# Optimization experiments

Measured on AMD Instinct MI355X. Metric: run time of the kernel, lower is better.

## Reference

```python
import jax, jax.numpy as jnp
import numpy as np

B, S, D, H = 1, 4096, 1024, 16
HD = D // H  # head_dim = 64
NEG = -1e9


def _rotate_half(x):
    x1, x2 = jnp.split(x, 2, axis=-1)
    return jnp.concatenate([-x2, x1], axis=-1)


def _apply_rope(x, cos, sin):
    # x: [b, s, h, hd]; cos/sin: [s, hd] -> broadcast over batch and heads
    c = cos[None, :, None, :]
    s = sin[None, :, None, :]
    return x * c + _rotate_half(x) * s


def setup_inputs() -> dict:
    key = jax.random.key(0)
    kx, kq, ko = jax.random.split(key, 3)
    x = jax.random.normal(kx, (B, S, D), dtype=jnp.float32)
    # causal additive mask (finite large-negative for safe grads)
    i = jnp.arange(S)
    attn_mask = jnp.where(i[None, :] > i[:, None], NEG, 0.0).astype(jnp.float32)[None, None]
    # standard RoPE tables
    inv_freq = 1.0 / (10000.0 ** (np.arange(0, HD, 2, dtype=np.float32) / HD))
    ang = np.arange(S, dtype=np.float32)[:, None] * inv_freq[None, :]  # [S, HD/2]
    ang = np.concatenate([ang, ang], axis=-1)  # [S, HD]
    rope_cos = jnp.asarray(np.cos(ang))
    rope_sin = jnp.asarray(np.sin(ang))
    W_qkv = jax.random.normal(kq, (D, 3 * D), dtype=jnp.float32) * (D ** -0.5)
    W_out = jax.random.normal(ko, (D, D), dtype=jnp.float32) * (D ** -0.5)
    return {"x": x, "attn_mask": attn_mask, "rope_cos": rope_cos,
            "rope_sin": rope_sin, "W_qkv": W_qkv, "W_out": W_out}


def reference(x, attn_mask, rope_cos, rope_sin, W_qkv, W_out):
    b, s, d = x.shape
    qkv = x @ W_qkv                              # [b, s, 3d]
    q, k, v = jnp.split(qkv, 3, axis=-1)
    q = q.reshape(b, s, H, HD)
    k = k.reshape(b, s, H, HD)
    v = v.reshape(b, s, H, HD)
    q = _apply_rope(q, rope_cos, rope_sin)
    k = _apply_rope(k, rope_cos, rope_sin)
    att = jnp.einsum('bqhd,bkhd->bhqk', q, k) / jnp.sqrt(jnp.float32(HD))
    att = att + attn_mask                        # additive mask broadcast [b,h,s,s]
    att = jax.nn.softmax(att, axis=-1)
    out = jnp.einsum('bhqk,bkhd->bqhd', att, v).reshape(b, s, d)
    return out @ W_out
```

## Files before the change

### kernel.cpp

```cpp
#include <hip/hip_runtime.h>


typedef __attribute__((ext_vector_type(8)))  __bf16 bf16x8;
typedef __attribute__((ext_vector_type(4)))  float  f32x4;
typedef __attribute__((ext_vector_type(16))) float  f32x16;
typedef __attribute__((ext_vector_type(8)))  unsigned short ushort8;
typedef __attribute__((ext_vector_type(4)))  unsigned int   u32x4;

#define MFMA16(a,b,c) __builtin_amdgcn_mfma_f32_16x16x32_bf16((a),(b),(c),0,0,0)
#define MFMA32(a,b,c) __builtin_amdgcn_mfma_f32_32x32x16_bf16((a),(b),(c),0,0,0)

static __device__ __forceinline__ unsigned short f2bf(float f) {
  unsigned int u = __builtin_bit_cast(unsigned int, f);
  u = (u + 0x7FFFu + ((u >> 16) & 1u)) >> 16;
  return (unsigned short)u;
}
static __device__ __forceinline__ float bf2f(unsigned short u) {
  return __builtin_bit_cast(float, (unsigned int)u << 16);
}
static __device__ __forceinline__ unsigned int cvtpk(float a, float b) {
  unsigned int r;
  asm("v_cvt_pk_bf16_f32 %0, %1, %2" : "=v"(r) : "v"(a), "v"(b));
  return r;
}
static __device__ __forceinline__ void plswap(unsigned int& a, unsigned int& b) {
#if __has_builtin(__builtin_amdgcn_permlane32_swap)
  auto r = __builtin_amdgcn_permlane32_swap(a, b, false, false);
  a = r[0]; b = r[1];
#else
  unsigned int xa = (unsigned int)__shfl_xor((int)a, 32);
  unsigned int xb = (unsigned int)__shfl_xor((int)b, 32);
  int lane = __builtin_amdgcn_mbcnt_hi(~0u, __builtin_amdgcn_mbcnt_lo(~0u, 0));
  bool hi = lane >= 32;
  a = hi ? xb : a;
  b = hi ? b : xa;
#endif
}
static __device__ __forceinline__ void gll16(const unsigned short* gp, const unsigned short* lp) {
  unsigned int m0v = __builtin_amdgcn_readfirstlane((unsigned int)(unsigned long long)(uintptr_t)lp);
  asm volatile("s_mov_b32 m0, %0\n\tglobal_load_lds_dwordx4 %1, off"
               :: "s"(m0v), "v"(gp) : "memory");
}
static __device__ __forceinline__ void wait_dma() {
  asm volatile("s_waitcnt vmcnt(0)" ::: "memory");
}

__global__ void convert_x(const float* __restrict__ x, unsigned short* __restrict__ o) {
  int i = (blockIdx.x * 256 + threadIdx.x) * 4;
  float4 v = *reinterpret_cast<const float4*>(x + i);
  ushort4 u;
  u.x = f2bf(v.x); u.y = f2bf(v.y); u.z = f2bf(v.z); u.w = f2bf(v.w);
  *reinterpret_cast<ushort4*>(o + i) = u;
}

__global__ void transpose_w(const float* __restrict__ W, unsigned short* __restrict__ WT,
                            int R, int C) {
  __shared__ float t[32][33];
  int c0 = blockIdx.x * 32, r0 = blockIdx.y * 32;
  int tx = threadIdx.x, ty = threadIdx.y;
#pragma unroll
  for (int i = 0; i < 32; i += 8)
    t[ty + i][tx] = W[(size_t)(r0 + ty + i) * C + c0 + tx];
  __syncthreads();
#pragma unroll
  for (int i = 0; i < 32; i += 8)
    WT[(size_t)(c0 + ty + i) * R + r0 + tx] = f2bf(t[tx][ty + i]);
}

template <typename OutT>
__global__ __launch_bounds__(256) void gemm_lds(const unsigned short* __restrict__ A,
                                                const unsigned short* __restrict__ BT,
                                                OutT* __restrict__ C, int M, int N, int K) {
  __shared__ __align__(16) unsigned short As[128 * 32];
  __shared__ __align__(16) unsigned short Bs[128 * 32];
  int tid = threadIdx.x;
  int lane = tid & 63, w = tid >> 6;
  int wr = w >> 1, wc = w & 1;
  int row0 = blockIdx.y * 128, col0 = blockIdx.x * 128;
  int lr = lane & 15, lk = lane >> 4;
  f32x4 acc[4][4] = {};
  for (int k0 = 0; k0 < K; k0 += 32) {
#pragma unroll
    for (int i = 0; i < 2; ++i) {
      int c = i * 256 + tid;
      int r = c >> 2, cc = (c & 3) * 8;
      gll16(A  + (size_t)(row0 + r) * K + k0 + cc, &As[i * 2048 + w * 512]);
      gll16(BT + (size_t)(col0 + r) * K + k0 + cc, &Bs[i * 2048 + w * 512]);
    }
    wait_dma();
    __syncthreads();
    bf16x8 a[4], b[4];
#pragma unroll
    for (int m = 0; m < 4; m++)
      a[m] = *reinterpret_cast<const bf16x8*>(&As[(wr * 64 + m * 16 + lr) * 32 + lk * 8]);
#pragma unroll
    for (int n = 0; n < 4; n++)
      b[n] = *reinterpret_cast<const bf16x8*>(&Bs[(wc * 64 + n * 16 + lr) * 32 + lk * 8]);
#pragma unroll
    for (int m = 0; m < 4; m++)
#pragma unroll
      for (int n = 0; n < 4; n++)
        acc[m][n] = MFMA16(a[m], b[n], acc[m][n]);
    __syncthreads();
  }
#pragma unroll
  for (int m = 0; m < 4; m++)
#pragma unroll
    for (int n = 0; n < 4; n++)
#pragma unroll
      for (int r = 0; r < 4; r++) {
        size_t off = (size_t)(row0 + wr * 64 + m * 16 + lk * 4 + r) * N + col0 + wc * 64 + n * 16 + lr;
        if constexpr (sizeof(OutT) == 2) C[off] = f2bf(acc[m][n][r]);
        else                             C[off] = acc[m][n][r];
      }
}

__global__ void rope_qk(const unsigned short* __restrict__ qkv,
                        const float* __restrict__ cosb, const float* __restrict__ sinb,
                        unsigned short* __restrict__ Q, unsigned short* __restrict__ K) {
  const float QSCALE = 0.125f * 1.4426950408889634f;
  int idx = blockIdx.x * 256 + threadIdx.x;
  int c = idx & 7, s = (idx >> 3) & 4095, h = idx >> 15;
  int d0 = c * 8;
  int base = s * 3072 + h * 64;
  ushort8 qv  = *reinterpret_cast<const ushort8*>(qkv + base + d0);
  ushort8 qv2 = *reinterpret_cast<const ushort8*>(qkv + base + (d0 ^ 32));
  ushort8 kv  = *reinterpret_cast<const ushort8*>(qkv + base + 1024 + d0);
  ushort8 kv2 = *reinterpret_cast<const ushort8*>(qkv + base + 1024 + (d0 ^ 32));
  float sign = (d0 < 32) ? -1.f : 1.f;
  const float4* cp = reinterpret_cast<const float4*>(cosb + s * 64 + d0);
  const float4* sp = reinterpret_cast<const float4*>(sinb + s * 64 + d0);
  float4 c0 = cp[0], c1 = cp[1], s0 = sp[0], s1 = sp[1];
  float co[8] = {c0.x, c0.y, c0.z, c0.w, c1.x, c1.y, c1.z, c1.w};
  float si[8] = {s0.x, s0.y, s0.z, s0.w, s1.x, s1.y, s1.z, s1.w};
  ushort8 qo, ko;
#pragma unroll
  for (int j = 0; j < 8; ++j) {
    float q = bf2f(qv[j]), q2 = bf2f(qv2[j]);
    float k = bf2f(kv[j]), k2 = bf2f(kv2[j]);
    qo[j] = f2bf((q * co[j] + sign * q2 * si[j]) * QSCALE);
    ko[j] = f2bf(k * co[j] + sign * k2 * si[j]);
  }
  *reinterpret_cast<ushort8*>(Q + (size_t)h * 262144 + (size_t)s * 64 + d0) = qo;
  int tt = s >> 5, ql = s & 31, lo = (d0 >> 3) & 1, f = d0 >> 4;
  size_t koff = (size_t)h * 262144 + (size_t)tt * 2048 + (size_t)f * 512
              + (size_t)(lo * 32 + ql) * 8;
  *reinterpret_cast<ushort8*>(K + koff) = ko;
}

__global__ __launch_bounds__(256) void v_frag_prep(const unsigned short* __restrict__ qkv,
                                                   unsigned short* __restrict__ VF) {
  __shared__ unsigned short tile[32][68];
  int t = blockIdx.x, h = blockIdx.y;
  int tid = threadIdx.x;
  {
    int r = tid >> 3, c8 = (tid & 7) * 8;
    *reinterpret_cast<ushort8*>(&tile[r][c8]) =
        *reinterpret_cast<const ushort8*>(qkv + (size_t)(t * 32 + r) * 3072 + 2048 + h * 64 + c8);
  }
  __syncthreads();
  int f = tid >> 6, lane = tid & 63;
  int ql = lane & 31, lo = lane >> 5;
  int sb = (f & 1) * 16 + lo * 8;
  int d  = (f >> 1) * 32 + ql;
  ushort8 v;
#pragma unroll
  for (int j = 0; j < 8; ++j) v[j] = tile[sb + j][d];
  *reinterpret_cast<ushort8*>(VF + (size_t)h * 262144 + (size_t)t * 2048
                              + (size_t)f * 512 + (size_t)lane * 8) = v;
}

__global__ __launch_bounds__(256) void flash_attn32(const unsigned short* __restrict__ Q,
                                                    const unsigned short* __restrict__ Kf,
                                                    const unsigned short* __restrict__ Vf,
                                                    unsigned short* __restrict__ O) {
  const int S = 4096;
  __shared__ __align__(16) unsigned short sbuf[2][4][2048];
  __shared__ float mrg[2][64][34];
  int flat = blockIdx.x;
  int virt = (flat & 7) * 64 + (flat >> 3);
  int h = virt >> 5;
  int i = virt & 31;
  int tid = threadIdx.x;
  int lane = tid & 63, w = tid >> 6;
  int qm = w & 1, pp = w >> 1;
  int ql = lane & 31, lo = lane >> 5;
  const unsigned short* Qh  = Q  + (size_t)h * S * 64;
  const unsigned short* KfH = Kf + (size_t)h * S * 64;
  const unsigned short* VfH = Vf + (size_t)h * S * 64;

  const unsigned short* img_src = (w & 1) ? VfH : KfH;
  int img_dt = w >> 1;
  auto stage = [&](int nb, int win) {
    int t = 2 * win + img_dt;
    const unsigned short* src = img_src + (size_t)t * 2048;
    const unsigned short* dst = &sbuf[nb][w][0];
#pragma unroll
    for (int j = 0; j < 4; ++j)
      gll16(src + j * 512 + lane * 8, dst + j * 512);
  };

  auto run_phase = [&](int base_qt) {
    int qt = base_qt + qm;
    int q0 = qt * 32;
    int nwin = base_qt / 2 + 1;
    bf16x8 qf[4];
#pragma unroll
    for (int f = 0; f < 4; ++f)
      qf[f] = *reinterpret_cast<const bf16x8*>(Qh + (q0 + ql) * 64 + f * 16 + lo * 8);
    f32x16 oT0 = {}, oT1 = {};
    float l = 0.f;

    stage(0, 0);
    wait_dma();
    __syncthreads();
    int cb = 0;
    for (int win = 0; win < nwin; ++win) {
      if (win + 1 < nwin) stage(cb ^ 1, win + 1);
      int t = 2 * win + pp;
      if (t <= qt) {
        const unsigned short* kb = &sbuf[cb][2 * pp][0];
        const unsigned short* vb = &sbuf[cb][2 * pp + 1][0];
        bf16x8 k0 = *reinterpret_cast<const bf16x8*>(kb);
        bf16x8 k1 = *reinterpret_cast<const bf16x8*>(kb + 512 + lane * 8 - lane * 8);
        k0 = *reinterpret_cast<const bf16x8*>(kb + 0 * 512 + lane * 8);
        k1 = *reinterpret_cast<const bf16x8*>(kb + 1 * 512 + lane * 8);
        bf16x8 k2 = *reinterpret_cast<const bf16x8*>(kb + 2 * 512 + lane * 8);
        bf16x8 k3 = *reinterpret_cast<const bf16x8*>(kb + 3 * 512 + lane * 8);
        f32x16 p = {};
        __builtin_amdgcn_s_setprio(1);
        p = MFMA32(k0, qf[0], p);
        p = MFMA32(k1, qf[1], p);
        p = MFMA32(k2, qf[2], p);
        p = MFMA32(k3, qf[3], p);
        __builtin_amdgcn_s_setprio(0);
        bf16x8 v00 = *reinterpret_cast<const bf16x8*>(vb + 0 * 512 + lane * 8);
        bf16x8 v01 = *reinterpret_cast<const bf16x8*>(vb + 1 * 512 + lane * 8);
        bf16x8 v10 = *reinterpret_cast<const bf16x8*>(vb + 2 * 512 + lane * 8);
        bf16x8 v11 = *reinterpret_cast<const bf16x8*>(vb + 3 * 512 + lane * 8);
        if (t == qt) {
#pragma unroll
          for (int r = 0; r < 16; ++r) {
            int kvr = (r & 3) + 8 * (r >> 2) + 4 * lo;
            if (kvr > ql) p[r] = -1e9f;
          }
        }
#pragma unroll
        for (int r = 0; r < 16; ++r) p[r] = __builtin_amdgcn_exp2f(p[r]);
        {
          float s0 = (p[0] + p[1])   + (p[2] + p[3]);
          float s1 = (p[4] + p[5])   + (p[6] + p[7]);
          float s2 = (p[8] + p[9])   + (p[10] + p[11]);
          float s3 = (p[12] + p[13]) + (p[14] + p[15]);
          l += (s0 + s1) + (s2 + s3);
        }
        unsigned int A0 = cvtpk(p[0],  p[1]),  A1 = cvtpk(p[2],  p[3]);
        unsigned int B0 = cvtpk(p[4],  p[5]),  B1 = cvtpk(p[6],  p[7]);
        plswap(A0, B0); plswap(A1, B1);
        u32x4 w0 = {A0, A1, B0, B1};
        bf16x8 P0 = __builtin_bit_cast(bf16x8, w0);
        unsigned int C0 = cvtpk(p[8],  p[9]),  C1 = cvtpk(p[10], p[11]);
        unsigned int D0 = cvtpk(p[12], p[13]), D1 = cvtpk(p[14], p[15]);
        plswap(C0, D0); plswap(C1, D1);
        u32x4 w1 = {C0, C1, D0, D1};
        bf16x8 P1 = __builtin_bit_cast(bf16x8, w1);
        __builtin_amdgcn_s_setprio(1);
        oT0 = MFMA32(v00, P0, oT0);
        oT1 = MFMA32(v10, P0, oT1);
        oT0 = MFMA32(v01, P1, oT0);
        oT1 = MFMA32(v11, P1, oT1);
        __builtin_amdgcn_s_setprio(0);
      }
      wait_dma();
      __syncthreads();
      cb ^= 1;
    }

    if (pp == 1) {
#pragma unroll
      for (int r = 0; r < 16; ++r) {
        mrg[qm][lane][r]      = oT0[r];
        mrg[qm][lane][16 + r] = oT1[r];
      }
      mrg[qm][lane][32] = l;
    }
    __syncthreads();
    if (pp == 0) {
#pragma unroll
      for (int r = 0; r < 16; ++r) {
        oT0[r] += mrg[qm][lane][r];
        oT1[r] += mrg[qm][lane][16 + r];
      }
      l += mrg[qm][lane][32];
      l += __shfl_xor(l, 32);
      float rl = 1.0f / l;
      size_t obase = (size_t)(q0 + ql) * 1024 + h * 64;
#pragma unroll
      for (int r = 0; r < 16; ++r) {
        int d = (r & 3) + 8 * (r >> 2) + 4 * lo;
        O[obase + d]      = f2bf(oT0[r] * rl);
        O[obase + 32 + d] = f2bf(oT1[r] * rl);
      }
    }
    __syncthreads();
  };

  run_phase(126 - 2 * i);
  run_phase(2 * i);
}

extern "C" void kernel_launch(void* const* d_in, const int* in_sizes, int n_in,
                              void* d_out, int out_size, void* d_ws, size_t ws_size,
                              hipStream_t stream) {
  const float* x        = (const float*)d_in[0];
  const float* rope_cos = (const float*)d_in[2];
  const float* rope_sin = (const float*)d_in[3];
  const float* W_qkv    = (const float*)d_in[4];
  const float* W_out    = (const float*)d_in[5];
  float* out = (float*)d_out;

  char* ws = (char*)d_ws;
  const size_t MB = 1u << 20;
  unsigned short* xbf   = (unsigned short*)(ws + 0 * MB);
  unsigned short* WqkvT = (unsigned short*)(ws + 8 * MB);
  unsigned short* WoutT = (unsigned short*)(ws + 14 * MB);
  unsigned short* qkv   = (unsigned short*)(ws + 16 * MB);
  unsigned short* Qb    = (unsigned short*)(ws + 40 * MB);
  unsigned short* Kfb   = (unsigned short*)(ws + 48 * MB);
  unsigned short* Vfb   = (unsigned short*)(ws + 56 * MB);
  unsigned short* Ob    = (unsigned short*)(ws + 64 * MB);

  convert_x<<<4096, 256, 0, stream>>>(x, xbf);
  transpose_w<<<dim3(3072 / 32, 1024 / 32), dim3(32, 8), 0, stream>>>(W_qkv, WqkvT, 1024, 3072);
  transpose_w<<<dim3(1024 / 32, 1024 / 32), dim3(32, 8), 0, stream>>>(W_out, WoutT, 1024, 1024);

  gemm_lds<unsigned short><<<dim3(3072 / 128, 4096 / 128), 256, 0, stream>>>(
      xbf, WqkvT, qkv, 4096, 3072, 1024);

  rope_qk<<<2048, 256, 0, stream>>>(qkv, rope_cos, rope_sin, Qb, Kfb);
  v_frag_prep<<<dim3(128, 16), 256, 0, stream>>>(qkv, Vfb);

  flash_attn32<<<512, 256, 0, stream>>>(Qb, Kfb, Vfb, Ob);

  gemm_lds<float><<<dim3(1024 / 128, 4096 / 128), 256, 0, stream>>>(
      Ob, WoutT, out, 4096, 1024, 1024);
}
```

Measured before the change: 147.9 us.

## Merge prep kernels and split attention phases into separate blocks

Result: faster. 142.2 us (-3.9%).

```diff
diff --git a/kernel.cpp b/kernel.cpp
--- a/kernel.cpp
+++ b/kernel.cpp
@@ -45,19 +45,32 @@
   asm volatile("s_waitcnt vmcnt(0)" ::: "memory");
 }
 
-__global__ void convert_x(const float* __restrict__ x, unsigned short* __restrict__ o) {
-  int i = (blockIdx.x * 256 + threadIdx.x) * 4;
-  float4 v = *reinterpret_cast<const float4*>(x + i);
-  ushort4 u;
-  u.x = f2bf(v.x); u.y = f2bf(v.y); u.z = f2bf(v.z); u.w = f2bf(v.w);
-  *reinterpret_cast<ushort4*>(o + i) = u;
-}
-
-__global__ void transpose_w(const float* __restrict__ W, unsigned short* __restrict__ WT,
-                            int R, int C) {
+__global__ __launch_bounds__(256) void prep_a(const float* __restrict__ x,
+                                              const float* __restrict__ W_qkv,
+                                              const float* __restrict__ W_out,
+                                              unsigned short* __restrict__ xbf,
+                                              unsigned short* __restrict__ WqkvT,
+                                              unsigned short* __restrict__ WoutT) {
   __shared__ float t[32][33];
-  int c0 = blockIdx.x * 32, r0 = blockIdx.y * 32;
-  int tx = threadIdx.x, ty = threadIdx.y;
+  int b = blockIdx.x, tid = threadIdx.x;
+  if (b < 4096) {
+    int i = (b * 256 + tid) * 4;
+    float4 v = *reinterpret_cast<const float4*>(x + i);
+    ushort4 u;
+    u.x = f2bf(v.x); u.y = f2bf(v.y); u.z = f2bf(v.z); u.w = f2bf(v.w);
+    *reinterpret_cast<ushort4*>(xbf + i) = u;
+    return;
+  }
+  const float* W; unsigned short* WT; int R, C, cx, ry;
+  if (b < 4096 + 3072) {
+    int idx = b - 4096; W = W_qkv; WT = WqkvT; R = 1024; C = 3072;
+    cx = idx % 96; ry = idx / 96;
+  } else {
+    int idx = b - 7168; W = W_out; WT = WoutT; R = 1024; C = 1024;
+    cx = idx % 32; ry = idx / 32;
+  }
+  int c0 = cx * 32, r0 = ry * 32;
+  int tx = tid & 31, ty = tid >> 5;
 #pragma unroll
   for (int i = 0; i < 32; i += 8)
     t[ty + i][tx] = W[(size_t)(r0 + ty + i) * C + c0 + tx];
@@ -115,44 +128,47 @@
       }
 }
 
-__global__ void rope_qk(const unsigned short* __restrict__ qkv,
-                        const float* __restrict__ cosb, const float* __restrict__ sinb,
-                        unsigned short* __restrict__ Q, unsigned short* __restrict__ K) {
-  const float QSCALE = 0.125f * 1.4426950408889634f;
-  int idx = blockIdx.x * 256 + threadIdx.x;
-  int c = idx & 7, s = (idx >> 3) & 4095, h = idx >> 15;
-  int d0 = c * 8;
-  int base = s * 3072 + h * 64;
-  ushort8 qv  = *reinterpret_cast<const ushort8*>(qkv + base + d0);
-  ushort8 qv2 = *reinterpret_cast<const ushort8*>(qkv + base + (d0 ^ 32));
-  ushort8 kv  = *reinterpret_cast<const ushort8*>(qkv + base + 1024 + d0);
-  ushort8 kv2 = *reinterpret_cast<const ushort8*>(qkv + base + 1024 + (d0 ^ 32));
-  float sign = (d0 < 32) ? -1.f : 1.f;
-  const float4* cp = reinterpret_cast<const float4*>(cosb + s * 64 + d0);
-  const float4* sp = reinterpret_cast<const float4*>(sinb + s * 64 + d0);
-  float4 c0 = cp[0], c1 = cp[1], s0 = sp[0], s1 = sp[1];
-  float co[8] = {c0.x, c0.y, c0.z, c0.w, c1.x, c1.y, c1.z, c1.w};
-  float si[8] = {s0.x, s0.y, s0.z, s0.w, s1.x, s1.y, s1.z, s1.w};
-  ushort8 qo, ko;
-#pragma unroll
-  for (int j = 0; j < 8; ++j) {
-    float q = bf2f(qv[j]), q2 = bf2f(qv2[j]);
-    float k = bf2f(kv[j]), k2 = bf2f(kv2[j]);
-    qo[j] = f2bf((q * co[j] + sign * q2 * si[j]) * QSCALE);
-    ko[j] = f2bf(k * co[j] + sign * k2 * si[j]);
-  }
-  *reinterpret_cast<ushort8*>(Q + (size_t)h * 262144 + (size_t)s * 64 + d0) = qo;
-  int tt = s >> 5, ql = s & 31, lo = (d0 >> 3) & 1, f = d0 >> 4;
-  size_t koff = (size_t)h * 262144 + (size_t)tt * 2048 + (size_t)f * 512
-              + (size_t)(lo * 32 + ql) * 8;
-  *reinterpret_cast<ushort8*>(K + koff) = ko;
-}
-
-__global__ __launch_bounds__(256) void v_frag_prep(const unsigned short* __restrict__ qkv,
-                                                   unsigned short* __restrict__ VF) {
+__global__ __launch_bounds__(256) void prep_b(const unsigned short* __restrict__ qkv,
+                                              const float* __restrict__ cosb,
+                                              const float* __restrict__ sinb,
+                                              unsigned short* __restrict__ Q,
+                                              unsigned short* __restrict__ K,
+                                              unsigned short* __restrict__ VF) {
   __shared__ unsigned short tile[32][68];
-  int t = blockIdx.x, h = blockIdx.y;
-  int tid = threadIdx.x;
+  int b = blockIdx.x, tid = threadIdx.x;
+  if (b < 2048) {
+    const float QSCALE = 0.125f * 1.4426950408889634f;
+    int idx = b * 256 + tid;
+    int c = idx & 7, s = (idx >> 3) & 4095, h = idx >> 15;
+    int d0 = c * 8;
+    int base = s * 3072 + h * 64;
+    ushort8 qv  = *reinterpret_cast<const ushort8*>(qkv + base + d0);
+    ushort8 qv2 = *reinterpret_cast<const ushort8*>(qkv + base + (d0 ^ 32));
+    ushort8 kv  = *reinterpret_cast<const ushort8*>(qkv + base + 1024 + d0);
+    ushort8 kv2 = *reinterpret_cast<const ushort8*>(qkv + base + 1024 + (d0 ^ 32));
+    float sign = (d0 < 32) ? -1.f : 1.f;
+    const float4* cp = reinterpret_cast<const float4*>(cosb + s * 64 + d0);
+    const float4* sp = reinterpret_cast<const float4*>(sinb + s * 64 + d0);
+    float4 c0 = cp[0], c1 = cp[1], s0 = sp[0], s1 = sp[1];
+    float co[8] = {c0.x, c0.y, c0.z, c0.w, c1.x, c1.y, c1.z, c1.w};
+    float si[8] = {s0.x, s0.y, s0.z, s0.w, s1.x, s1.y, s1.z, s1.w};
+    ushort8 qo, ko;
+#pragma unroll
+    for (int j = 0; j < 8; ++j) {
+      float q = bf2f(qv[j]), q2 = bf2f(qv2[j]);
+      float k = bf2f(kv[j]), k2 = bf2f(kv2[j]);
+      qo[j] = f2bf((q * co[j] + sign * q2 * si[j]) * QSCALE);
+      ko[j] = f2bf(k * co[j] + sign * k2 * si[j]);
+    }
+    *reinterpret_cast<ushort8*>(Q + (size_t)h * 262144 + (size_t)s * 64 + d0) = qo;
+    int tt = s >> 5, ql = s & 31, lo = (d0 >> 3) & 1, f = d0 >> 4;
+    size_t koff = (size_t)h * 262144 + (size_t)tt * 2048 + (size_t)f * 512
+                + (size_t)(lo * 32 + ql) * 8;
+    *reinterpret_cast<ushort8*>(K + koff) = ko;
+    return;
+  }
+  int vb = b - 2048;
+  int t = vb & 127, h = vb >> 7;
   {
     int r = tid >> 3, c8 = (tid & 7) * 8;
     *reinterpret_cast<ushort8*>(&tile[r][c8]) =
@@ -176,11 +192,13 @@
                                                     unsigned short* __restrict__ O) {
   const int S = 4096;
   __shared__ __align__(16) unsigned short sbuf[2][4][2048];
-  __shared__ float mrg[2][64][34];
+  __shared__ float lmrg[2][64];
   int flat = blockIdx.x;
-  int virt = (flat & 7) * 64 + (flat >> 3);
-  int h = virt >> 5;
-  int i = virt & 31;
+  int xcd = flat & 7;
+  int v = flat >> 3;
+  int h2 = v >> 6, a = (v >> 5) & 1, u = v & 31;
+  int h = xcd * 2 + h2;
+  int base = a ? (2 * u) : (126 - 2 * u);
   int tid = threadIdx.x;
   int lane = tid & 63, w = tid >> 6;
   int qm = w & 1, pp = w >> 1;
@@ -200,113 +218,105 @@
       gll16(src + j * 512 + lane * 8, dst + j * 512);
   };
 
-  auto run_phase = [&](int base_qt) {
-    int qt = base_qt + qm;
-    int q0 = qt * 32;
-    int nwin = base_qt / 2 + 1;
-    bf16x8 qf[4];
-#pragma unroll
-    for (int f = 0; f < 4; ++f)
-      qf[f] = *reinterpret_cast<const bf16x8*>(Qh + (q0 + ql) * 64 + f * 16 + lo * 8);
-    f32x16 oT0 = {}, oT1 = {};
-    float l = 0.f;
-
-    stage(0, 0);
+  int qt = base + qm;
+  int q0 = qt * 32;
+  int nwin = base / 2 + 1;
+  bf16x8 qf[4];
+#pragma unroll
+  for (int f = 0; f < 4; ++f)
+    qf[f] = *reinterpret_cast<const bf16x8*>(Qh + (q0 + ql) * 64 + f * 16 + lo * 8);
+  f32x16 oT0 = {}, oT1 = {};
+  float l = 0.f;
+
+  stage(0, 0);
+  wait_dma();
+  __syncthreads();
+  int cb = 0;
+  for (int win = 0; win < nwin; ++win) {
+    if (win + 1 < nwin) stage(cb ^ 1, win + 1);
+    int t = 2 * win + pp;
+    if (t <= qt) {
+      const unsigned short* kb = &sbuf[cb][2 * pp][0];
+      const unsigned short* vb = &sbuf[cb][2 * pp + 1][0];
+      bf16x8 k0 = *reinterpret_cast<const bf16x8*>(kb + 0 * 512 + lane * 8);
+      bf16x8 k1 = *reinterpret_cast<const bf16x8*>(kb + 1 * 512 + lane * 8);
+      bf16x8 k2 = *reinterpret_cast<const bf16x8*>(kb + 2 * 512 + lane * 8);
+      bf16x8 k3 = *reinterpret_cast<const bf16x8*>(kb + 3 * 512 + lane * 8);
+      f32x16 p = {};
+      __builtin_amdgcn_s_setprio(1);
+      p = MFMA32(k0, qf[0], p);
+      p = MFMA32(k1, qf[1], p);
+      p = MFMA32(k2, qf[2], p);
+      p = MFMA32(k3, qf[3], p);
+      __builtin_amdgcn_s_setprio(0);
+      bf16x8 v00 = *reinterpret_cast<const bf16x8*>(vb + 0 * 512 + lane * 8);
+      bf16x8 v01 = *reinterpret_cast<const bf16x8*>(vb + 1 * 512 + lane * 8);
+      bf16x8 v10 = *reinterpret_cast<const bf16x8*>(vb + 2 * 512 + lane * 8);
+      bf16x8 v11 = *reinterpret_cast<const bf16x8*>(vb + 3 * 512 + lane * 8);
+      if (t == qt) {
+#pragma unroll
+        for (int r = 0; r < 16; ++r) {
+          int kvr = (r & 3) + 8 * (r >> 2) + 4 * lo;
+          if (kvr > ql) p[r] = -1e9f;
+        }
+      }
+#pragma unroll
+      for (int r = 0; r < 16; ++r) p[r] = __builtin_amdgcn_exp2f(p[r]);
+      {
+        float s0 = (p[0] + p[1])   + (p[2] + p[3]);
+        float s1 = (p[4] + p[5])   + (p[6] + p[7]);
+        float s2 = (p[8] + p[9])   + (p[10] + p[11]);
+        float s3 = (p[12] + p[13]) + (p[14] + p[15]);
+        l += (s0 + s1) + (s2 + s3);
+      }
+      unsigned int A0 = cvtpk(p[0],  p[1]),  A1 = cvtpk(p[2],  p[3]);
+      unsigned int B0 = cvtpk(p[4],  p[5]),  B1 = cvtpk(p[6],  p[7]);
+      plswap(A0, B0); plswap(A1, B1);
+      u32x4 w0 = {A0, A1, B0, B1};
+      bf16x8 P0 = __builtin_bit_cast(bf16x8, w0);
+      unsigned int C0 = cvtpk(p[8],  p[9]),  C1 = cvtpk(p[10], p[11]);
+      unsigned int D0 = cvtpk(p[12], p[13]), D1 = cvtpk(p[14], p[15]);
+      plswap(C0, D0); plswap(C1, D1);
+      u32x4 w1 = {C0, C1, D0, D1};
+      bf16x8 P1 = __builtin_bit_cast(bf16x8, w1);
+      __builtin_amdgcn_s_setprio(1);
+      oT0 = MFMA32(v00, P0, oT0);
+      oT1 = MFMA32(v10, P0, oT1);
+      oT0 = MFMA32(v01, P1, oT0);
+      oT1 = MFMA32(v11, P1, oT1);
+      __builtin_amdgcn_s_setprio(0);
+    }
     wait_dma();
     __syncthreads();
-    int cb = 0;
-    for (int win = 0; win < nwin; ++win) {
-      if (win + 1 < nwin) stage(cb ^ 1, win + 1);
-      int t = 2 * win + pp;
-      if (t <= qt) {
-        const unsigned short* kb = &sbuf[cb][2 * pp][0];
-        const unsigned short* vb = &sbuf[cb][2 * pp + 1][0];
-        bf16x8 k0 = *reinterpret_cast<const bf16x8*>(kb);
-        bf16x8 k1 = *reinterpret_cast<const bf16x8*>(kb + 512 + lane * 8 - lane * 8);
-        k0 = *reinterpret_cast<const bf16x8*>(kb + 0 * 512 + lane * 8);
-        k1 = *reinterpret_cast<const bf16x8*>(kb + 1 * 512 + lane * 8);
-        bf16x8 k2 = *reinterpret_cast<const bf16x8*>(kb + 2 * 512 + lane * 8);
-        bf16x8 k3 = *reinterpret_cast<const bf16x8*>(kb + 3 * 512 + lane * 8);
-        f32x16 p = {};
-        __builtin_amdgcn_s_setprio(1);
-        p = MFMA32(k0, qf[0], p);
-        p = MFMA32(k1, qf[1], p);
-        p = MFMA32(k2, qf[2], p);
-        p = MFMA32(k3, qf[3], p);
-        __builtin_amdgcn_s_setprio(0);
-        bf16x8 v00 = *reinterpret_cast<const bf16x8*>(vb + 0 * 512 + lane * 8);
-        bf16x8 v01 = *reinterpret_cast<const bf16x8*>(vb + 1 * 512 + lane * 8);
-        bf16x8 v10 = *reinterpret_cast<const bf16x8*>(vb + 2 * 512 + lane * 8);
-        bf16x8 v11 = *reinterpret_cast<const bf16x8*>(vb + 3 * 512 + lane * 8);
-        if (t == qt) {
-#pragma unroll
-          for (int r = 0; r < 16; ++r) {
-            int kvr = (r & 3) + 8 * (r >> 2) + 4 * lo;
-            if (kvr > ql) p[r] = -1e9f;
-          }
-        }
-#pragma unroll
-        for (int r = 0; r < 16; ++r) p[r] = __builtin_amdgcn_exp2f(p[r]);
-        {
-          float s0 = (p[0] + p[1])   + (p[2] + p[3]);
-          float s1 = (p[4] + p[5])   + (p[6] + p[7]);
-          float s2 = (p[8] + p[9])   + (p[10] + p[11]);
-          float s3 = (p[12] + p[13]) + (p[14] + p[15]);
-          l += (s0 + s1) + (s2 + s3);
-        }
-        unsigned int A0 = cvtpk(p[0],  p[1]),  A1 = cvtpk(p[2],  p[3]);
-        unsigned int B0 = cvtpk(p[4],  p[5]),  B1 = cvtpk(p[6],  p[7]);
-        plswap(A0, B0); plswap(A1, B1);
-        u32x4 w0 = {A0, A1, B0, B1};
-        bf16x8 P0 = __builtin_bit_cast(bf16x8, w0);
-        unsigned int C0 = cvtpk(p[8],  p[9]),  C1 = cvtpk(p[10], p[11]);
-        unsigned int D0 = cvtpk(p[12], p[13]), D1 = cvtpk(p[14], p[15]);
-        plswap(C0, D0); plswap(C1, D1);
-        u32x4 w1 = {C0, C1, D0, D1};
-        bf16x8 P1 = __builtin_bit_cast(bf16x8, w1);
-        __builtin_amdgcn_s_setprio(1);
-        oT0 = MFMA32(v00, P0, oT0);
-        oT1 = MFMA32(v10, P0, oT1);
-        oT0 = MFMA32(v01, P1, oT0);
-        oT1 = MFMA32(v11, P1, oT1);
-        __builtin_amdgcn_s_setprio(0);
-      }
-      wait_dma();
-      __syncthreads();
-      cb ^= 1;
-    }
-
-    if (pp == 1) {
-#pragma unroll
-      for (int r = 0; r < 16; ++r) {
-        mrg[qm][lane][r]      = oT0[r];
-        mrg[qm][lane][16 + r] = oT1[r];
-      }
-      mrg[qm][lane][32] = l;
-    }
-    __syncthreads();
-    if (pp == 0) {
-#pragma unroll
-      for (int r = 0; r < 16; ++r) {
-        oT0[r] += mrg[qm][lane][r];
-        oT1[r] += mrg[qm][lane][16 + r];
-      }
-      l += mrg[qm][lane][32];
-      l += __shfl_xor(l, 32);
-      float rl = 1.0f / l;
-      size_t obase = (size_t)(q0 + ql) * 1024 + h * 64;
-#pragma unroll
-      for (int r = 0; r < 16; ++r) {
-        int d = (r & 3) + 8 * (r >> 2) + 4 * lo;
-        O[obase + d]      = f2bf(oT0[r] * rl);
-        O[obase + 32 + d] = f2bf(oT1[r] * rl);
-      }
-    }
-    __syncthreads();
-  };
-
-  run_phase(126 - 2 * i);
-  run_phase(2 * i);
+    cb ^= 1;
+  }
+
+  float* fm = reinterpret_cast<float*>(&sbuf[0][0][0]);
+  if (pp == 1) {
+    float* dst = fm + (qm * 64 + lane) * 33;
+#pragma unroll
+    for (int r = 0; r < 16; ++r) { dst[r] = oT0[r]; dst[16 + r] = oT1[r]; }
+    lmrg[qm][lane] = l;
+  }
+  __syncthreads();
+  if (pp == 0) {
+    const float* src = fm + (qm * 64 + lane) * 33;
+#pragma unroll
+    for (int r = 0; r < 16; ++r) {
+      oT0[r] += src[r];
+      oT1[r] += src[16 + r];
+    }
+    l += lmrg[qm][lane];
+    l += __shfl_xor(l, 32);
+    float rl = 1.0f / l;
+    size_t obase = (size_t)(q0 + ql) * 1024 + h * 64;
+#pragma unroll
+    for (int r = 0; r < 16; ++r) {
+      int d = (r & 3) + 8 * (r >> 2) + 4 * lo;
+      O[obase + d]      = f2bf(oT0[r] * rl);
+      O[obase + 32 + d] = f2bf(oT1[r] * rl);
+    }
+  }
 }
 
 extern "C" void kernel_launch(void* const* d_in, const int* in_sizes, int n_in,
@@ -330,17 +340,14 @@
   unsigned short* Vfb   = (unsigned short*)(ws + 56 * MB);
   unsigned short* Ob    = (unsigned short*)(ws + 64 * MB);
 
-  convert_x<<<4096, 256, 0, stream>>>(x, xbf);
-  transpose_w<<<dim3(3072 / 32, 1024 / 32), dim3(32, 8), 0, stream>>>(W_qkv, WqkvT, 1024, 3072);
-  transpose_w<<<dim3(1024 / 32, 1024 / 32), dim3(32, 8), 0, stream>>>(W_out, WoutT, 1024, 1024);
+  prep_a<<<8192, 256, 0, stream>>>(x, W_qkv, W_out, xbf, WqkvT, WoutT);
 
   gemm_lds<unsigned short><<<dim3(3072 / 128, 4096 / 128), 256, 0, stream>>>(
       xbf, WqkvT, qkv, 4096, 3072, 1024);
 
-  rope_qk<<<2048, 256, 0, stream>>>(qkv, rope_cos, rope_sin, Qb, Kfb);
-  v_frag_prep<<<dim3(128, 16), 256, 0, stream>>>(qkv, Vfb);
-
-  flash_attn32<<<512, 256, 0, stream>>>(Qb, Kfb, Vfb, Ob);
+  prep_b<<<4096, 256, 0, stream>>>(qkv, rope_cos, rope_sin, Qb, Kfb, Vfb);
+
+  flash_attn32<<<1024, 256, 0, stream>>>(Qb, Kfb, Vfb, Ob);
 
   gemm_lds<float><<<dim3(1024 / 128, 4096 / 128), 256, 0, stream>>>(
       Ob, WoutT, out, 4096, 1024, 1024);
```
